# Performance work log

Measured on AMD Instinct MI355X. Metric: run time of the kernel, lower is better.

## Reference

```python
import jax, jax.numpy as jnp
import numpy as np
import math

B, L, E, H, NL, M, S, R = 4, 1024, 512, 8, 2, 2048, 256, 2
Dh = E // H
NEG = jnp.finfo(jnp.float32).min


def _posenc(n, d):
    pos = np.arange(n)[:, None].astype(np.float32)
    div = np.exp(np.arange(0, d, 2).astype(np.float32) * (-math.log(10000.0) / d))
    pe = np.zeros((n, d), np.float32)
    pe[:, 0::2] = np.sin(pos * div)
    pe[:, 1::2] = np.cos(pos * div)
    return jnp.asarray(pe)


def _temb(t, dim, max_positions=10000):
    half = dim // 2
    freqs = jnp.exp(jnp.arange(half, dtype=jnp.float32) * (-math.log(max_positions) / (half - 1)))
    a = t[:, None] * freqs[None, :]
    return jnp.concatenate([jnp.sin(a), jnp.cos(a)], axis=1)


def _ln(x, s, b, eps=1e-5):
    m = x.mean(-1, keepdims=True)
    v = jnp.mean((x - m) ** 2, axis=-1, keepdims=True)
    return (x - m) * jax.lax.rsqrt(v + eps) * s + b


def _gelu(x):
    return jax.nn.gelu(x, approximate=False)


def _block(h, W, b, lns, lnb, mW1, mb1, mW2, mb2, mask):
    # prenorm self-attention
    z = _ln(h, lns[0], lnb[0])
    q = (z @ W[0] + b[0]).reshape(B, L, H, Dh) / math.sqrt(Dh)
    k = (z @ W[1] + b[1]).reshape(B, L, H, Dh)
    v = (z @ W[2] + b[2]).reshape(B, L, H, Dh)
    logits = jnp.einsum('bqhd,bkhd->bhqk', q, k)
    att = jax.nn.softmax(jnp.where(mask, logits, NEG), axis=-1)
    o = jnp.einsum('bhqk,bkhd->bqhd', att, v).reshape(B, L, E)
    h = h + o @ W[3] + b[3]
    # prenorm feed-forward
    z = _ln(h, lns[1], lnb[1])
    return h + _gelu(z @ mW1 + mb1) @ mW2 + mb2


def setup_inputs():
    key = jax.random.key(0)
    ks = iter(jax.random.split(key, 48))
    def nrm(shape, s=0.02):
        return jax.random.normal(next(ks), shape, jnp.float32) * s
    inp = {
        'x': jax.random.randint(next(ks), (B, L), 0, S),
        't': jax.random.uniform(next(ks), (B,), jnp.float32) * 1000.0,
        'embed': nrm((S, E), 1.0),
        'attn_W': nrm((2, NL, 4, E, E)),
        'attn_b': jnp.zeros((2, NL, 4, E)),
        'ln_s': jnp.ones((2, NL, 2, E)),
        'ln_b': jnp.zeros((2, NL, 2, E)),
        'mlp_W1': nrm((2, NL, E, M)),
        'mlp_b1': jnp.zeros((2, NL, M)),
        'mlp_W2': nrm((2, NL, M, E)),
        'mlp_b2': jnp.zeros((2, NL, E)),
        'ca_Wq': nrm((E, E)),
        'ca_Wk': nrm((E, E)), 'ca_bk': jnp.zeros((E,)),
        'ca_Wv': nrm((E, E)), 'ca_bv': jnp.zeros((E,)),
        'ca_Wo': nrm((E, E)), 'ca_bo': jnp.zeros((E,)),
        'ro_ln1_s': jnp.ones((E,)), 'ro_ln1_b': jnp.zeros((E,)),
        'ro_ln2_s': jnp.ones((E,)), 'ro_ln2_b': jnp.zeros((E,)),
        'in_W': nrm((E, 2 * E)), 'in_b': jnp.zeros((2 * E,)),
        'tmlp_W1': nrm((E, M)), 'tmlp_b1': jnp.zeros((M,)),
        'tmlp_W2': nrm((M, 4 * E)), 'tmlp_b2': jnp.zeros((4 * E,)),
        'res_W1': nrm((R, 2 * E, M)), 'res_b1': jnp.zeros((R, M)),
        'res_W2': nrm((R, M, 2 * E)), 'res_b2': jnp.zeros((R, 2 * E)),
        'res_ln_s': jnp.ones((R, 2 * E)), 'res_ln_b': jnp.zeros((R, 2 * E)),
        'film_W': nrm((R, 4 * E, 4 * E)), 'film_b': jnp.ones((R, 4 * E)),
        'out_W': nrm((2 * E, S)), 'out_b': jnp.zeros((S,)),
    }
    return inp


def reference(x, t, embed, attn_W, attn_b, ln_s, ln_b, mlp_W1, mlp_b1, mlp_W2, mlp_b2,
              ca_Wq, ca_Wk, ca_bk, ca_Wv, ca_bv, ca_Wo, ca_bo,
              ro_ln1_s, ro_ln1_b, ro_ln2_s, ro_ln2_b,
              in_W, in_b, tmlp_W1, tmlp_b1, tmlp_W2, tmlp_b2,
              res_W1, res_b1, res_W2, res_b2, res_ln_s, res_ln_b,
              film_W, film_b, out_W, out_b):
    temb = _temb(t, E)                       # [B,E]
    tok = embed[x]                           # [B,L,E]
    pe = _posenc(L, E)[None]
    cond = temb[:, None, :]
    il = jnp.arange(L)
    causal = (il[None, :] <= il[:, None])[None, None]  # [1,1,L,L]
    embeds = []
    for d in range(2):
        if d == 0:  # l2r: shift right, prepend temb token, causal mask
            h = jnp.concatenate([cond, tok[:, :-1]], axis=1)
            mask = causal
        else:       # r2l: shift left, append temb token, anti-causal mask
            h = jnp.concatenate([tok[:, 1:], cond], axis=1)
            mask = jnp.swapaxes(causal, -1, -2)
        h = h + pe
        for l in range(NL):
            h = _block(h, attn_W[d, l], attn_b[d, l], ln_s[d, l], ln_b[d, l],
                       mlp_W1[d, l], mlp_b1[d, l], mlp_W2[d, l], mlp_b2[d, l], mask)
        embeds.append(h)
    l2r_embed, r2l_embed = embeds
    # AttentionReadout (prenorm) with joint-mask cross-attention
    inputs = l2r_embed + r2l_embed
    l2r_n = _ln(l2r_embed, ro_ln1_s, ro_ln1_b)
    r2l_n = _ln(r2l_embed, ro_ln2_s, ro_ln2_b)
    q = ((l2r_n + r2l_n) @ ca_Wq).reshape(B, L, H, Dh) / math.sqrt(Dh)
    allv = jnp.concatenate([temb[:, None], l2r_n, r2l_n], axis=1)  # [B,2L+1,E]
    k = (allv @ ca_Wk + ca_bk).reshape(B, 2 * L + 1, H, Dh)
    v = (allv @ ca_Wv + ca_bv).reshape(B, 2 * L + 1, H, Dh)
    logits = jnp.einsum('bqhd,bkhd->bhqk', q, k)  # [B,H,L,2L+1]
    m_l2r = il[None, :] > il[:, None]   # triu, diag=1
    m_r2l = il[None, :] < il[:, None]   # tril, diag=-1
    joint = jnp.concatenate([jnp.ones((L, 1), bool), m_l2r, m_r2l], axis=-1)[None, None]
    att = jax.nn.softmax(jnp.where(joint, logits, NEG), axis=-1)
    xat = jnp.einsum('bhqk,bkhd->bqhd', att, v).reshape(B, L, E)
    xat = xat @ ca_Wo + ca_bo + inputs
    # ResidualReadout: FiLM-conditioned residual MLP stack
    t4 = _gelu(temb @ tmlp_W1 + tmlp_b1) @ tmlp_W2 + tmlp_b2  # [B,4E]
    h = xat @ in_W + in_b                                     # [B,L,2E]
    for i in range(R):
        film = t4 @ film_W[i] + film_b[i]
        z = _gelu(h @ res_W1[i] + res_b1[i]) @ res_W2[i] + res_b2[i]
        h = _ln(h + z, res_ln_s[i], res_ln_b[i])
        fa, fb = jnp.split(film[:, None, :], 2, axis=-1)
        h = fa * h + fb
    return h @ out_W + out_b  # [B,L,S]
```

## Files before the change

kernel.cpp:

```cpp
#include <hip/hip_runtime.h>
#include <hip/hip_bf16.h>


#define NEGF -3.4028235e38f
#define LOG2E 1.4426950408889634f

using bf16x8 = __attribute__((ext_vector_type(8))) short;
using f32x4  = __attribute__((ext_vector_type(4))) float;

__device__ inline float bf2f(unsigned short u) {
    return __uint_as_float(((unsigned int)u) << 16);
}
__device__ inline unsigned short f2b(float f) {
    unsigned int u = __float_as_uint(f);
    return (unsigned short)((u + 0x7fff + ((u >> 16) & 1)) >> 16);
}

__device__ inline void gl_lds16(const void* g, void* l) {
    __builtin_amdgcn_global_load_lds(
        (const __attribute__((address_space(1))) void*)(uintptr_t)g,
        (__attribute__((address_space(3))) void*)(unsigned int)(uintptr_t)l,
        16, 0, 0);
}

template<int BM>
__global__ __launch_bounds__(256) void gemm_bf16_k(
    const unsigned short* __restrict__ A,
    const unsigned short* __restrict__ Wt0, const unsigned short* __restrict__ Wt1,
    const float* __restrict__ bias0, const float* __restrict__ bias1, int mhalf,
    const float* __restrict__ res,
    float* __restrict__ Cf, unsigned short* __restrict__ Cb,
    unsigned short* __restrict__ CbK, unsigned short* __restrict__ Ct, int ldkv,
    int M, int N, int K, float alpha, int gelu_flag, int qkv)
{
    constexpr int MF  = BM / 32;
    constexpr int NAC = BM * 4 / 256;
    __shared__ unsigned short As[2][BM * 32];
    __shared__ unsigned short Bs[2][4096];
    const int tid  = threadIdx.x;
    const int wid  = tid >> 6;
    const int lane = tid & 63;
    const int wy   = wid >> 1, wx = wid & 1;
    const int koff = lane >> 4, l16 = lane & 15;
    const int m0 = blockIdx.y * BM, n0 = blockIdx.x * 128;

    const unsigned short* Wt = (m0 < mhalf) ? Wt0 : Wt1;
    const float* bias = (m0 < mhalf) ? bias0 : bias1;

    const unsigned short* aG[NAC];
    const unsigned short* bG[2];
    #pragma unroll
    for (int i = 0; i < NAC; ++i) {
        int c = tid + i * 256;
        int r = ((c >> 6) << 4) | (c & 15), kk = ((c >> 4) & 3) << 3;
        aG[i] = A + (size_t)(m0 + r) * K + kk;
    }
    #pragma unroll
    for (int i = 0; i < 2; ++i) {
        int c = tid + i * 256;
        int r = ((c >> 6) << 4) | (c & 15), kk = ((c >> 4) & 3) << 3;
        bG[i] = Wt + (size_t)(n0 + r) * K + kk;
    }

    f32x4 acc[MF][4] = {};
    const int nk = K >> 5;

    auto stage = [&](int buf, int k0) {
        #pragma unroll
        for (int i = 0; i < NAC; ++i)
            gl_lds16(aG[i] + k0, &As[buf][(size_t)(i * 256 + wid * 64) * 8]);
        #pragma unroll
        for (int i = 0; i < 2; ++i)
            gl_lds16(bG[i] + k0, &Bs[buf][(size_t)(i * 256 + wid * 64) * 8]);
    };

    stage(0, 0);
    int cur = 0;
    for (int it = 0; it < nk; ++it) {
        if (it + 1 < nk) {
            stage(cur ^ 1, (it + 1) << 5);
            if constexpr (BM == 128)
                asm volatile("s_waitcnt vmcnt(4)" ::: "memory");
            else
                asm volatile("s_waitcnt vmcnt(3)" ::: "memory");
        } else {
            asm volatile("s_waitcnt vmcnt(0)" ::: "memory");
        }
        __builtin_amdgcn_s_barrier();

        bf16x8 af[MF], bfr[4];
        const int foff = (koff * 16 + l16) * 8;
        #pragma unroll
        for (int i = 0; i < MF; ++i)
            af[i] = *(const bf16x8*)&As[cur][(size_t)((wy * MF + i) * 64) * 8 + foff];
        #pragma unroll
        for (int j = 0; j < 4; ++j)
            bfr[j] = *(const bf16x8*)&Bs[cur][(size_t)((wx * 4 + j) * 64) * 8 + foff];
        #pragma unroll
        for (int i = 0; i < MF; ++i)
            #pragma unroll
            for (int j = 0; j < 4; ++j)
                acc[i][j] = __builtin_amdgcn_mfma_f32_16x16x32_bf16(
                    af[i], bfr[j], acc[i][j], 0, 0, 0);

        asm volatile("" ::: "memory");
        __builtin_amdgcn_s_barrier();
        cur ^= 1;
    }

    #pragma unroll
    for (int i = 0; i < MF; ++i) {
        const int rbase = m0 + wy * (MF * 16) + i * 16 + koff * 4;
        #pragma unroll
        for (int j = 0; j < 4; ++j) {
            const int gn = n0 + wx * 64 + j * 16 + l16;
            const float bs = bias ? bias[gn] : 0.f;
            if (qkv) {
                const int seg = gn >> 9, gnl = gn & 511;
                const float av = (seg == 0) ? 0.125f : 1.0f;
                unsigned short o[4];
                #pragma unroll
                for (int r = 0; r < 4; ++r) o[r] = f2b((acc[i][j][r] + bs) * av);
                if (seg == 0) {
                    #pragma unroll
                    for (int r = 0; r < 4; ++r)
                        Cb[(size_t)(rbase + r) * 512 + gnl] = o[r];
                } else if (seg == 1) {
                    #pragma unroll
                    for (int r = 0; r < 4; ++r)
                        CbK[(size_t)(rbase + r) * 512 + gnl] = o[r];
                } else {
                    const int hh = gnl >> 6, dh = gnl & 63;
                    const int bb = rbase >> 10, l0 = rbase & 1023;
                    *(ushort4*)(Ct + ((size_t)(bb * 8 + hh) * 64 + dh) * 1024 + l0) =
                        make_ushort4(o[0], o[1], o[2], o[3]);
                }
            } else {
                float vr[4];
                #pragma unroll
                for (int r = 0; r < 4; ++r) {
                    float v = (acc[i][j][r] + bs) * alpha;
                    if (gelu_flag) v = 0.5f * v * (1.0f + erff(v * 0.70710678118654752f));
                    const size_t idx = (size_t)(rbase + r) * N + gn;
                    if (res) v += res[idx];
                    if (Cf) Cf[idx] = v;
                    if (Cb) Cb[idx] = f2b(v);
                    vr[r] = v;
                }
                if (Ct) {
                    const int hh = gn >> 6, dh = gn & 63;
                    const int bb = rbase / ldkv;
                    const int l0 = rbase - bb * ldkv;
                    *(ushort4*)(Ct + ((size_t)(bb * 8 + hh) * 64 + dh) * ldkv + l0) =
                        make_ushort4(f2b(vr[0]), f2b(vr[1]), f2b(vr[2]), f2b(vr[3]));
                }
            }
        }
    }
}

__global__ __launch_bounds__(256) void wconv(
    const float* __restrict__ src, unsigned short* __restrict__ dst,
    int K, int N, long sstride, long dstride)
{
    __shared__ float t[64][65];
    const int n0 = blockIdx.x * 64, k0 = blockIdx.y * 64;
    const float* s = src + (size_t)blockIdx.z * sstride;
    unsigned short* d = dst + (size_t)blockIdx.z * dstride;
    const int tid = threadIdx.x;
    #pragma unroll
    for (int i = 0; i < 4; ++i) {
        int lin = i * 1024 + tid * 4;
        int r = lin >> 6, c = lin & 63;
        float4 v = *(const float4*)(s + (size_t)(k0 + r) * N + n0 + c);
        t[r][c] = v.x; t[r][c + 1] = v.y; t[r][c + 2] = v.z; t[r][c + 3] = v.w;
    }
    __syncthreads();
    #pragma unroll
    for (int i = 0; i < 8; ++i) {
        int lin = i * 512 + tid * 2;
        int rn = lin >> 6, ck = lin & 63;
        ushort2 o;
        o.x = f2b(t[ck][rn]); o.y = f2b(t[ck + 1][rn]);
        *(ushort2*)(d + (size_t)(n0 + rn) * K + k0 + ck) = o;
    }
}

__global__ __launch_bounds__(256) void skinny_k(
    const float* __restrict__ A, const float* __restrict__ W,
    float* __restrict__ P, int N, int K)
{
    const int n = blockIdx.x * 256 + threadIdx.x;
    const int s = blockIdx.y;
    const int k0 = s * 32;
    float a0 = 0.f, a1 = 0.f, a2 = 0.f, a3 = 0.f;
    #pragma unroll 8
    for (int k = k0; k < k0 + 32; ++k) {
        float w = W[(size_t)k * N + n];
        a0 = fmaf(A[k], w, a0);
        a1 = fmaf(A[K + k], w, a1);
        a2 = fmaf(A[2 * K + k], w, a2);
        a3 = fmaf(A[3 * K + k], w, a3);
    }
    float* p = P + (size_t)s * 4 * N;
    p[n] = a0; p[N + n] = a1; p[2 * N + n] = a2; p[3 * N + n] = a3;
}

__global__ __launch_bounds__(256) void skinny_red(
    const float* __restrict__ P, const float* __restrict__ bias,
    float* __restrict__ C, int N, int nsplit, int gelu_flag)
{
    const int n = blockIdx.x * 256 + threadIdx.x;
    const int r = blockIdx.y;
    float acc = 0.f;
    for (int s = 0; s < nsplit; ++s) acc += P[((size_t)s * 4 + r) * N + n];
    float v = acc + (bias ? bias[n] : 0.f);
    if (gelu_flag) v = 0.5f * v * (1.0f + erff(v * 0.70710678118654752f));
    C[(size_t)r * N + n] = v;
}

__global__ __launch_bounds__(256) void ln_kernel(
    const float* __restrict__ X, const float* __restrict__ X2,
    const float* __restrict__ s, const float* __restrict__ b,
    float* __restrict__ Yf, unsigned short* __restrict__ Yb,
    int D, const float* __restrict__ film, int rows_per_batch, long pstride)
{
    const int row = blockIdx.x;
    const int tid = threadIdx.x;
    const float* x = X + (size_t)row * D;
    const float* x2 = X2 ? X2 + (size_t)row * D : nullptr;
    const float* se = s + (size_t)(row >> 12) * pstride;
    const float* be = b + (size_t)(row >> 12) * pstride;

    float sum = 0.f, sq = 0.f;
    for (int c = tid; c < D; c += 256) {
        float v = x[c] + (x2 ? x2[c] : 0.f);
        sum += v; sq += v * v;
    }
    __shared__ float r1[4], r2[4];
    __shared__ float s_mean, s_rstd;
    for (int off = 32; off > 0; off >>= 1) {
        sum += __shfl_down(sum, off);
        sq  += __shfl_down(sq,  off);
    }
    if ((tid & 63) == 0) { r1[tid >> 6] = sum; r2[tid >> 6] = sq; }
    __syncthreads();
    if (tid == 0) {
        float ts = r1[0] + r1[1] + r1[2] + r1[3];
        float tq = r2[0] + r2[1] + r2[2] + r2[3];
        float mean = ts / (float)D;
        float var = tq / (float)D - mean * mean;
        s_mean = mean;
        s_rstd = rsqrtf(var + 1e-5f);
    }
    __syncthreads();
    const float mean = s_mean, rstd = s_rstd;
    const float* fa = nullptr; const float* fb = nullptr;
    if (film) {
        int batch = row / rows_per_batch;
        fa = film + (size_t)batch * 2 * D;
        fb = fa + D;
    }
    for (int c = tid; c < D; c += 256) {
        float v = x[c] + (x2 ? x2[c] : 0.f);
        float y = (v - mean) * rstd * se[c] + be[c];
        if (film) y = fa[c] * y + fb[c];
        if (Yf) Yf[(size_t)row * D + c] = y;
        if (Yb) Yb[(size_t)row * D + c] = f2b(y);
    }
}

__global__ void temb_kernel(const float* __restrict__ t, float* __restrict__ temb,
                            unsigned short* __restrict__ tembb)
{
    int b = blockIdx.x;
    int i = threadIdx.x;
    float f = expf((float)i * (-9.210340371976184f / 255.0f));
    float a = t[b] * f;
    float sv = sinf(a), cv = cosf(a);
    temb[b * 512 + i]        = sv;
    temb[b * 512 + 256 + i]  = cv;
    tembb[b * 512 + i]       = f2b(sv);
    tembb[b * 512 + 256 + i] = f2b(cv);
}

__global__ void embed_kernel(const int* __restrict__ x, const float* __restrict__ temb,
                             const float* __restrict__ embed,
                             float* __restrict__ l2r, float* __restrict__ r2l)
{
    const int i = blockIdx.x;
    const int b = blockIdx.y;
    const int d = blockIdx.z;
    float* out = (d == 0 ? l2r : r2l) + ((size_t)(b * 1024 + i) * 512);
    const float* src;
    if (d == 0) src = (i == 0)    ? temb + b * 512 : embed + (size_t)x[b * 1024 + (i - 1)] * 512;
    else        src = (i == 1023) ? temb + b * 512 : embed + (size_t)x[b * 1024 + (i + 1)] * 512;
    for (int e = threadIdx.x; e < 512; e += 256) {
        int j = e >> 1;
        float div = expf((float)(2 * j) * (-9.210340371976184f / 512.0f));
        float ang = (float)i * div;
        float pe = (e & 1) ? cosf(ang) : sinf(ang);
        out[e] = src[e] + pe;
    }
}

__global__ void add_kernel(const float* __restrict__ A, const float* __restrict__ B,
                           float* __restrict__ C, int n)
{
    int i = blockIdx.x * blockDim.x + threadIdx.x;
    int stride = gridDim.x * blockDim.x;
    for (; i < n; i += stride) C[i] = A[i] + B[i];
}

__global__ void add_bf16(const unsigned int* __restrict__ A,
                         const unsigned int* __restrict__ B,
                         unsigned int* __restrict__ C, int nwords)
{
    int i = blockIdx.x * blockDim.x + threadIdx.x;
    int stride = gridDim.x * blockDim.x;
    for (; i < nwords; i += stride) {
        unsigned int a = A[i], b = B[i];
        float lo = __uint_as_float(a << 16) + __uint_as_float(b << 16);
        float hi = __uint_as_float(a & 0xffff0000u) + __uint_as_float(b & 0xffff0000u);
        C[i] = (unsigned int)f2b(lo) | ((unsigned int)f2b(hi) << 16);
    }
}

__global__ void build_allv_b(const unsigned short* __restrict__ tembb,
                             const unsigned short* __restrict__ l2rn,
                             const unsigned short* __restrict__ r2ln,
                             unsigned short* __restrict__ allv)
{
    const int k = blockIdx.x;
    const int b = blockIdx.y;
    unsigned short* out = allv + ((size_t)b * 2080 + k) * 512;
    const unsigned short* src;
    if (k == 0)         src = tembb + b * 512;
    else if (k <= 1024) src = l2rn + ((size_t)(b * 1024 + (k - 1)) * 512);
    else                src = r2ln + ((size_t)(b * 1024 + (k - 1025)) * 512);
    ((uint4*)out)[threadIdx.x] = ((const uint4*)src)[threadIdx.x];
}

__global__ __launch_bounds__(256) void attn_mfma(
    const unsigned short* __restrict__ Q, const unsigned short* __restrict__ K,
    const unsigned short* __restrict__ Vt, unsigned short* __restrict__ O, int mode)
{
    const int E = 512;
    const int LKP = (mode == 2) ? 2080 : 1024;
    const int idf = blockIdx.x;
    const int chunk = gridDim.x >> 3;
    const int w = (idf & 7) * chunk + (idf >> 3);
    const int qt = w & 15, h = (w >> 4) & 7, bb = w >> 7;
    const int dir = (mode == 2) ? 2 : (bb >> 2);
    const int q0 = qt * 64;
    const int tid = threadIdx.x;
    const int wid = tid >> 6, lane = tid & 63;
    const int fr = lane & 15;
    const int fs = lane >> 4;
    const int wq0 = q0 + wid * 16;

    __shared__ unsigned short Qs[4096];
    __shared__ unsigned short Ks[4096];
    __shared__ unsigned short Vs[4096];
    __shared__ unsigned short Ps[4][16][72];

    {
        const unsigned short* Qbase = Q + ((size_t)bb * 1024 + q0) * E + h * 64;
        #pragma unroll
        for (int it = 0; it < 2; ++it) {
            int i = tid + it * 256;
            int r = i & 63, c = i >> 6;
            *(uint4*)&Qs[(size_t)(c * 64 + r) * 8] =
                *(const uint4*)(Qbase + (size_t)r * E + c * 8);
        }
    }
    __syncthreads();
    const bf16x8 aq0 = *(const bf16x8*)&Qs[(size_t)(fs * 64 + wid * 16 + fr) * 8];
    const bf16x8 aq1 = *(const bf16x8*)&Qs[(size_t)((fs + 4) * 64 + wid * 16 + fr) * 8];

    float m_r[4], l_r[4];
    f32x4 o_acc[4] = {};
    #pragma unroll
    for (int r = 0; r < 4; ++r) { m_r[r] = NEGF; l_r[r] = 0.f; }

    int kt0, kt1;
    if (dir == 0)      { kt0 = 0;  kt1 = qt; }
    else if (dir == 1) { kt0 = qt; kt1 = 15; }
    else               { kt0 = 0;  kt1 = 31; }

    const unsigned short* Kb0 = K + ((size_t)bb * LKP) * E + h * 64;
    const unsigned short* Vb0 = Vt + (size_t)(bb * 8 + h) * 64 * LKP;

    for (int kt = kt0; kt <= kt1; ++kt) {
        if (dir == 2) {
            if (kt >= 1 && kt <= 15 && 64 * kt + 62 <= q0) continue;
            if (kt >= 17 && 64 * kt - 1025 >= q0 + 63) continue;
        }
        const int k0 = kt * 64;

        __syncthreads();

        {
            const unsigned short* Kbase = Kb0 + (size_t)k0 * E;
            const unsigned short* Vbase = Vb0 + k0;
            #pragma unroll
            for (int it = 0; it < 2; ++it) {
                int i = tid + it * 256;
                int r = i & 63, c = i >> 6;
                *(uint4*)&Ks[(size_t)(c * 64 + r) * 8] =
                    *(const uint4*)(Kbase + (size_t)r * E + c * 8);
                *(uint4*)&Vs[(size_t)(c * 64 + r) * 8] =
                    *(const uint4*)(Vbase + (size_t)r * LKP + c * 8);
            }
        }
        __syncthreads();

        f32x4 s[4] = {};
        __builtin_amdgcn_s_setprio(1);
        #pragma unroll
        for (int t = 0; t < 4; ++t) {
            bf16x8 bk0 = *(const bf16x8*)&Ks[(size_t)(fs * 64 + t * 16 + fr) * 8];
            bf16x8 bk1 = *(const bf16x8*)&Ks[(size_t)((fs + 4) * 64 + t * 16 + fr) * 8];
            s[t] = __builtin_amdgcn_mfma_f32_16x16x32_bf16(aq0, bk0, s[t], 0, 0, 0);
            s[t] = __builtin_amdgcn_mfma_f32_16x16x32_bf16(aq1, bk1, s[t], 0, 0, 0);
        }
        __builtin_amdgcn_s_setprio(0);

        bool need_mask;
        if (dir != 2) need_mask = (kt == qt);
        else if (kt >= 1 && kt <= 15) need_mask = !((64 * kt - 1) > (q0 + 63));
        else if (kt >= 17)            need_mask = !((64 * kt + 63 - 1025) < q0);
        else                          need_mask = true;
        if (need_mask) {
            #pragma unroll
            for (int t = 0; t < 4; ++t) {
                #pragma unroll
                for (int r = 0; r < 4; ++r) {
                    int q = wq0 + fs * 4 + r;
                    int k = k0 + t * 16 + fr;
                    bool valid;
                    if (dir == 0)      valid = (k <= q);
                    else if (dir == 1) valid = (k >= q);
                    else valid = (k == 0) || (k <= 1024 ? (k - 1) > q : (k - 1025) < q);
                    if (!valid) s[t][r] = NEGF;
                }
            }
        }

        float c_[4], rs[4];
        #pragma unroll
        for (int r = 0; r < 4; ++r) {
            float v = fmaxf(fmaxf(s[0][r], s[1][r]), fmaxf(s[2][r], s[3][r]));
            v = fmaxf(v, __shfl_xor(v, 1));
            v = fmaxf(v, __shfl_xor(v, 2));
            v = fmaxf(v, __shfl_xor(v, 4));
            v = fmaxf(v, __shfl_xor(v, 8));
            float mnew = fmaxf(m_r[r], v);
            c_[r] = exp2f((m_r[r] - mnew) * LOG2E);
            m_r[r] = mnew;
            rs[r] = 0.f;
        }
        #pragma unroll
        for (int t = 0; t < 4; ++t) {
            #pragma unroll
            for (int r = 0; r < 4; ++r) {
                float p = exp2f((s[t][r] - m_r[r]) * LOG2E);
                s[t][r] = p;
                rs[r] += p;
            }
        }
        #pragma unroll
        for (int r = 0; r < 4; ++r) {
            float v = rs[r];
            v += __shfl_xor(v, 1);
            v += __shfl_xor(v, 2);
            v += __shfl_xor(v, 4);
            v += __shfl_xor(v, 8);
            l_r[r] = l_r[r] * c_[r] + v;
            o_acc[0][r] *= c_[r]; o_acc[1][r] *= c_[r];
            o_acc[2][r] *= c_[r]; o_acc[3][r] *= c_[r];
        }

        #pragma unroll
        for (int t = 0; t < 4; ++t)
            #pragma unroll
            for (int r = 0; r < 4; ++r)
                Ps[wid][fs * 4 + r][t * 16 + fr] = f2b(s[t][r]);
        __syncthreads();

        bf16x8 pa0 = *(const bf16x8*)&Ps[wid][fr][fs * 8];
        bf16x8 pa1 = *(const bf16x8*)&Ps[wid][fr][fs * 8 + 32];
        __builtin_amdgcn_s_setprio(1);
        #pragma unroll
        for (int t = 0; t < 4; ++t) {
            bf16x8 bv0 = *(const bf16x8*)&Vs[(size_t)(fs * 64 + t * 16 + fr) * 8];
            bf16x8 bv1 = *(const bf16x8*)&Vs[(size_t)((fs + 4) * 64 + t * 16 + fr) * 8];
            o_acc[t] = __builtin_amdgcn_mfma_f32_16x16x32_bf16(pa0, bv0, o_acc[t], 0, 0, 0);
            o_acc[t] = __builtin_amdgcn_mfma_f32_16x16x32_bf16(pa1, bv1, o_acc[t], 0, 0, 0);
        }
        __builtin_amdgcn_s_setprio(0);
    }

    unsigned short* Obase = O + ((size_t)bb * 1024 + q0) * E + h * 64;
    float invl[4];
    #pragma unroll
    for (int r = 0; r < 4; ++r) invl[r] = 1.f / l_r[r];
    #pragma unroll
    for (int t = 0; t < 4; ++t)
        #pragma unroll
        for (int r = 0; r < 4; ++r)
            Obase[(size_t)(wid * 16 + fs * 4 + r) * E + t * 16 + fr] =
                f2b(o_acc[t][r] * invl[r]);
}


static inline void gemmb(hipStream_t st, int BM, const unsigned short* A,
                         const unsigned short* Wt0, const unsigned short* Wt1,
                         const float* bias0, const float* bias1, int mhalf,
                         const float* res, float* Cf, unsigned short* Cb,
                         unsigned short* CbK, unsigned short* Ct, int ldkv,
                         int M, int N, int K, float alpha, int gelu, int qkv)
{
    dim3 g(N / 128, M / BM);
    if (BM == 128)
        gemm_bf16_k<128><<<g, dim3(256), 0, st>>>(A, Wt0, Wt1, bias0, bias1, mhalf,
            res, Cf, Cb, CbK, Ct, ldkv, M, N, K, alpha, gelu, qkv);
    else
        gemm_bf16_k<64><<<g, dim3(256), 0, st>>>(A, Wt0, Wt1, bias0, bias1, mhalf,
            res, Cf, Cb, CbK, Ct, ldkv, M, N, K, alpha, gelu, qkv);
}

static inline void sgemm4(hipStream_t st, const float* A, const float* W,
                          const float* bias, float* C, float* P,
                          int N, int K, int gelu)
{
    const int nsplit = K / 32;
    skinny_k<<<dim3(N / 256, nsplit), 256, 0, st>>>(A, W, P, N, K);
    skinny_red<<<dim3(N / 256, 4), 256, 0, st>>>(P, bias, C, N, nsplit, gelu);
}

extern "C" void kernel_launch(void* const* d_in, const int* in_sizes, int n_in,
                              void* d_out, int out_size, void* d_ws, size_t ws_size,
                              hipStream_t stream)
{
    const int*   x      = (const int*)  d_in[0];
    const float* t      = (const float*)d_in[1];
    const float* embedW = (const float*)d_in[2];
    const float* attn_W = (const float*)d_in[3];
    const float* attn_b = (const float*)d_in[4];
    const float* ln_s   = (const float*)d_in[5];
    const float* ln_b   = (const float*)d_in[6];
    const float* mlp_W1 = (const float*)d_in[7];
    const float* mlp_b1 = (const float*)d_in[8];
    const float* mlp_W2 = (const float*)d_in[9];
    const float* mlp_b2 = (const float*)d_in[10];
    const float* ca_Wq  = (const float*)d_in[11];
    const float* ca_Wk  = (const float*)d_in[12];
    const float* ca_bk  = (const float*)d_in[13];
    const float* ca_Wv  = (const float*)d_in[14];
    const float* ca_bv  = (const float*)d_in[15];
    const float* ca_Wo  = (const float*)d_in[16];
    const float* ca_bo  = (const float*)d_in[17];
    const float* ro1s   = (const float*)d_in[18];
    const float* ro1b   = (const float*)d_in[19];
    const float* ro2s   = (const float*)d_in[20];
    const float* ro2b   = (const float*)d_in[21];
    const float* in_W   = (const float*)d_in[22];
    const float* in_b   = (const float*)d_in[23];
    const float* tm_W1  = (const float*)d_in[24];
    const float* tm_b1  = (const float*)d_in[25];
    const float* tm_W2  = (const float*)d_in[26];
    const float* tm_b2  = (const float*)d_in[27];
    const float* res_W1 = (const float*)d_in[28];
    const float* res_b1 = (const float*)d_in[29];
    const float* res_W2 = (const float*)d_in[30];
    const float* res_b2 = (const float*)d_in[31];
    const float* rls    = (const float*)d_in[32];
    const float* rlb    = (const float*)d_in[33];
    const float* film_W = (const float*)d_in[34];
    const float* film_b = (const float*)d_in[35];
    const float* out_W  = (const float*)d_in[36];
    const float* out_b  = (const float*)d_in[37];
    float* out = (float*)d_out;
    (void)ws_size; (void)in_sizes; (void)n_in; (void)out_size;

    char* base = (char*)d_ws;
    size_t off = 0;
    auto alloc = [&](size_t bytes) -> char* {
        char* p = base + off;
        off = (off + bytes + 255) & ~(size_t)255;
        return p;
    };
    float* TEMB  = (float*)alloc(8192);
    float* TM1   = (float*)alloc(32768);
    float* T4    = (float*)alloc(32768);
    float* FILM  = (float*)alloc(32768);
    unsigned short* TEMBb = (unsigned short*)alloc(4096);
    float* SKP   = (float*)alloc(2097152);

    float* HB  = (float*)alloc(16777216);
    float* L2R = HB;
    float* R2L = HB + 4096 * 512;
    float* Z   = (float*)alloc(8388608);
    float* H2  = (float*)alloc(16777216);
    float* Z2  = (float*)alloc(16777216);

    unsigned short* Zb  = (unsigned short*)alloc(8388608);
    unsigned short* Qb  = (unsigned short*)alloc(8388608);
    unsigned short* Kb  = (unsigned short*)alloc(8388608);
    unsigned short* Vb  = (unsigned short*)alloc(8388608);
    unsigned short* Ob  = (unsigned short*)alloc(8388608);
    unsigned short* H2b = (unsigned short*)alloc(8388608);

    unsigned short* BIG = (unsigned short*)alloc(33554432);
    unsigned short* MIDb  = BIG;
    unsigned short* ALLVb = BIG;
    unsigned short* K2b   = BIG + 4259840;
    unsigned short* V2T   = BIG + 8519680;

    unsigned short* WT = (unsigned short*)alloc(45613056);
    const size_t wt_attn = 0,        wt_mlp1 = 4194304, wt_mlp2 = 8388608;
    const size_t wt_caq = 12582912,  wt_cak = 12845056, wt_cav = 13107200,
                 wt_cao = 13369344,  wt_in  = 13631488;
    const size_t wt_res1 = 14155776, wt_res2 = 18350080, wt_out = 22544384;

    wconv<<<dim3(8, 8, 16), 256, 0, stream>>>(attn_W, WT + wt_attn, 512, 512, 262144, 262144);
    wconv<<<dim3(32, 8, 4), 256, 0, stream>>>(mlp_W1, WT + wt_mlp1, 512, 2048, 1048576, 1048576);
    wconv<<<dim3(8, 32, 4), 256, 0, stream>>>(mlp_W2, WT + wt_mlp2, 2048, 512, 1048576, 1048576);
    wconv<<<dim3(8, 8), 256, 0, stream>>>(ca_Wq, WT + wt_caq, 512, 512, 0, 0);
    wconv<<<dim3(8, 8), 256, 0, stream>>>(ca_Wk, WT + wt_cak, 512, 512, 0, 0);
    wconv<<<dim3(8, 8), 256, 0, stream>>>(ca_Wv, WT + wt_cav, 512, 512, 0, 0);
    wconv<<<dim3(8, 8), 256, 0, stream>>>(ca_Wo, WT + wt_cao, 512, 512, 0, 0);
    wconv<<<dim3(16, 8), 256, 0, stream>>>(in_W, WT + wt_in, 512, 1024, 0, 0);
    wconv<<<dim3(32, 16, 2), 256, 0, stream>>>(res_W1, WT + wt_res1, 1024, 2048, 2097152, 2097152);
    wconv<<<dim3(16, 32, 2), 256, 0, stream>>>(res_W2, WT + wt_res2, 2048, 1024, 2097152, 2097152);
    wconv<<<dim3(4, 16), 256, 0, stream>>>(out_W, WT + wt_out, 1024, 256, 0, 0);

    temb_kernel<<<dim3(4), dim3(256), 0, stream>>>(t, TEMB, TEMBb);
    embed_kernel<<<dim3(1024, 4, 2), dim3(256), 0, stream>>>(x, TEMB, embedW, L2R, R2L);

    for (int l = 0; l < 2; ++l) {
        const size_t d1 = 2 + l;
        ln_kernel<<<8192, 256, 0, stream>>>(HB, nullptr,
            ln_s + (l * 2 + 0) * 512, ln_b + (l * 2 + 0) * 512,
            nullptr, Zb, 512, nullptr, 1024, 2048);
        gemmb(stream, 64, Zb,
              WT + wt_attn + (size_t)l * 1048576, WT + wt_attn + d1 * 1048576,
              attn_b + l * 2048, attn_b + d1 * 2048, 4096,
              nullptr, nullptr, Qb, Kb, Vb, 1024, 8192, 1536, 512, 1.f, 0, 1);
        attn_mfma<<<dim3(1024), dim3(256), 0, stream>>>(Qb, Kb, Vb, Ob, -1);
        gemmb(stream, 64, Ob,
              WT + wt_attn + (size_t)(l * 4 + 3) * 262144,
              WT + wt_attn + (d1 * 4 + 3) * 262144,
              attn_b + (l * 4 + 3) * 512, attn_b + (d1 * 4 + 3) * 512, 4096,
              HB, HB, nullptr, nullptr, nullptr, 1, 8192, 512, 512, 1.f, 0, 0);
        ln_kernel<<<8192, 256, 0, stream>>>(HB, nullptr,
            ln_s + (l * 2 + 1) * 512, ln_b + (l * 2 + 1) * 512,
            nullptr, Zb, 512, nullptr, 1024, 2048);
        gemmb(stream, 64, Zb,
              WT + wt_mlp1 + (size_t)l * 1048576, WT + wt_mlp1 + d1 * 1048576,
              mlp_b1 + l * 2048, mlp_b1 + d1 * 2048, 4096,
              nullptr, nullptr, MIDb, nullptr, nullptr, 1, 8192, 2048, 512, 1.f, 1, 0);
        gemmb(stream, 64, MIDb,
              WT + wt_mlp2 + (size_t)l * 1048576, WT + wt_mlp2 + d1 * 1048576,
              mlp_b2 + l * 512, mlp_b2 + d1 * 512, 4096,
              HB, HB, nullptr, nullptr, nullptr, 1, 8192, 512, 2048, 1.f, 0, 0);
    }

    add_kernel<<<2048, 256, 0, stream>>>(L2R, R2L, Z, 2097152);
    ln_kernel<<<4096, 256, 0, stream>>>(L2R, nullptr, ro1s, ro1b, nullptr, Qb, 512, nullptr, 1024, 0);
    ln_kernel<<<4096, 256, 0, stream>>>(R2L, nullptr, ro2s, ro2b, nullptr, Kb, 512, nullptr, 1024, 0);
    add_bf16<<<1024, 256, 0, stream>>>((const unsigned int*)Qb, (const unsigned int*)Kb,
                                       (unsigned int*)Vb, 1048576);
    build_allv_b<<<dim3(2049, 4), 64, 0, stream>>>(TEMBb, Qb, Kb, ALLVb);
    gemmb(stream, 64, Vb, WT + wt_caq, WT + wt_caq, nullptr, nullptr, 1 << 30,
          nullptr, nullptr, Zb, nullptr, nullptr, 1, 4096, 512, 512, 0.125f, 0, 0);
    gemmb(stream, 64, ALLVb, WT + wt_cak, WT + wt_cak, ca_bk, ca_bk, 1 << 30,
          nullptr, nullptr, K2b, nullptr, nullptr, 1, 8320, 512, 512, 1.f, 0, 0);
    gemmb(stream, 64, ALLVb, WT + wt_cav, WT + wt_cav, ca_bv, ca_bv, 1 << 30,
          nullptr, nullptr, nullptr, nullptr, V2T, 2080, 8320, 512, 512, 1.f, 0, 0);
    attn_mfma<<<dim3(512), dim3(256), 0, stream>>>(Zb, K2b, V2T, Ob, 2);
    gemmb(stream, 64, Ob, WT + wt_cao, WT + wt_cao, ca_bo, ca_bo, 1 << 30,
          Z, nullptr, Qb, nullptr, nullptr, 1, 4096, 512, 512, 1.f, 0, 0);

    sgemm4(stream, TEMB, tm_W1, tm_b1, TM1, SKP, 2048, 512, 1);
    sgemm4(stream, TM1, tm_W2, tm_b2, T4, SKP, 2048, 2048, 0);

    gemmb(stream, 64, Qb, WT + wt_in, WT + wt_in, in_b, in_b, 1 << 30,
          nullptr, H2, H2b, nullptr, nullptr, 1, 4096, 1024, 512, 1.f, 0, 0);
    for (int i = 0; i < 2; ++i) {
        sgemm4(stream, T4, film_W + (size_t)i * 4194304, film_b + i * 2048,
               FILM, SKP, 2048, 2048, 0);
        gemmb(stream, 64, H2b, WT + wt_res1 + (size_t)i * 2097152,
              WT + wt_res1 + (size_t)i * 2097152,
              res_b1 + i * 2048, res_b1 + i * 2048, 1 << 30,
              nullptr, nullptr, MIDb, nullptr, nullptr, 1, 4096, 2048, 1024, 1.f, 1, 0);
        gemmb(stream, 64, MIDb, WT + wt_res2 + (size_t)i * 2097152,
              WT + wt_res2 + (size_t)i * 2097152,
              res_b2 + i * 1024, res_b2 + i * 1024, 1 << 30,
              nullptr, Z2, nullptr, nullptr, nullptr, 1, 4096, 1024, 2048, 1.f, 0, 0);
        ln_kernel<<<4096, 256, 0, stream>>>(H2, Z2, rls + i * 1024, rlb + i * 1024,
                                            H2, H2b, 1024, FILM, 1024, 0);
    }

    gemmb(stream, 64, H2b, WT + wt_out, WT + wt_out, out_b, out_b, 1 << 30,
          nullptr, out, nullptr, nullptr, nullptr, 1, 4096, 256, 1024, 1.f, 0, 0);
}
```

Baseline: 1.136 ms.

## Triple-buffer GEMM LDS stages and register-prefetch attention K/V tiles

```diff
diff --git a/kernel.cpp b/kernel.cpp
--- a/kernel.cpp
+++ b/kernel.cpp
@@ -35,8 +35,8 @@
 {
     constexpr int MF  = BM / 32;
     constexpr int NAC = BM * 4 / 256;
-    __shared__ unsigned short As[2][BM * 32];
-    __shared__ unsigned short Bs[2][4096];
+    __shared__ unsigned short As[3][BM * 32];
+    __shared__ unsigned short Bs[3][4096];
     const int tid  = threadIdx.x;
     const int wid  = tid >> 6;
     const int lane = tid & 63;
@@ -75,16 +75,19 @@
     };
 
     stage(0, 0);
-    int cur = 0;
+    if (nk > 1) stage(1, 32);
+    int cur = 0, nxt = 2;
     for (int it = 0; it < nk; ++it) {
-        if (it + 1 < nk) {
-            stage(cur ^ 1, (it + 1) << 5);
-            if constexpr (BM == 128)
-                asm volatile("s_waitcnt vmcnt(4)" ::: "memory");
-            else
-                asm volatile("s_waitcnt vmcnt(3)" ::: "memory");
+        const int ahead = nk - 1 - it;
+        if (ahead >= 2) stage(nxt, (it + 2) << 5);
+        if constexpr (BM == 128) {
+            if (ahead >= 2)      asm volatile("s_waitcnt vmcnt(8)" ::: "memory");
+            else if (ahead == 1) asm volatile("s_waitcnt vmcnt(4)" ::: "memory");
+            else                 asm volatile("s_waitcnt vmcnt(0)" ::: "memory");
         } else {
-            asm volatile("s_waitcnt vmcnt(0)" ::: "memory");
+            if (ahead >= 2)      asm volatile("s_waitcnt vmcnt(6)" ::: "memory");
+            else if (ahead == 1) asm volatile("s_waitcnt vmcnt(3)" ::: "memory");
+            else                 asm volatile("s_waitcnt vmcnt(0)" ::: "memory");
         }
         __builtin_amdgcn_s_barrier();
 
@@ -105,7 +108,8 @@
 
         asm volatile("" ::: "memory");
         __builtin_amdgcn_s_barrier();
-        cur ^= 1;
+        cur = (cur == 2) ? 0 : cur + 1;
+        nxt = (nxt == 2) ? 0 : nxt + 1;
     }
 
     #pragma unroll
@@ -383,37 +387,49 @@
     #pragma unroll
     for (int r = 0; r < 4; ++r) { m_r[r] = NEGF; l_r[r] = 0.f; }
 
-    int kt0, kt1;
-    if (dir == 0)      { kt0 = 0;  kt1 = qt; }
-    else if (dir == 1) { kt0 = qt; kt1 = 15; }
-    else               { kt0 = 0;  kt1 = 31; }
+    int nt, ktA = 1;
+    if (dir == 0)      nt = qt + 1;
+    else if (dir == 1) nt = 16 - qt;
+    else { ktA = (qt >= 1) ? qt : 1; nt = 1 + (qt + 16 - ktA + 1); }
+    auto kt_of = [&](int j) -> int {
+        if (dir == 0) return j;
+        if (dir == 1) return qt + j;
+        return (j == 0) ? 0 : (ktA + j - 1);
+    };
 
     const unsigned short* Kb0 = K + ((size_t)bb * LKP) * E + h * 64;
     const unsigned short* Vb0 = Vt + (size_t)(bb * 8 + h) * 64 * LKP;
 
-    for (int kt = kt0; kt <= kt1; ++kt) {
-        if (dir == 2) {
-            if (kt >= 1 && kt <= 15 && 64 * kt + 62 <= q0) continue;
-            if (kt >= 17 && 64 * kt - 1025 >= q0 + 63) continue;
-        }
+    const int sr = tid & 63, sc = tid >> 6;
+    auto load_tile = [&](int kt, uint4* kr, uint4* vr) {
+        const unsigned short* Kbase = Kb0 + (size_t)(kt * 64) * E;
+        const unsigned short* Vbase = Vb0 + kt * 64;
+        #pragma unroll
+        for (int it = 0; it < 2; ++it) {
+            kr[it] = *(const uint4*)(Kbase + (size_t)sr * E + (sc + it * 4) * 8);
+            vr[it] = *(const uint4*)(Vbase + (size_t)sr * LKP + (sc + it * 4) * 8);
+        }
+    };
+
+    uint4 kr[2], vr[2];
+    load_tile(kt_of(0), kr, vr);
+
+    for (int j = 0; j < nt; ++j) {
+        const int kt = kt_of(j);
         const int k0 = kt * 64;
 
-        __syncthreads();
-
-        {
-            const unsigned short* Kbase = Kb0 + (size_t)k0 * E;
-            const unsigned short* Vbase = Vb0 + k0;
-            #pragma unroll
-            for (int it = 0; it < 2; ++it) {
-                int i = tid + it * 256;
-                int r = i & 63, c = i >> 6;
-                *(uint4*)&Ks[(size_t)(c * 64 + r) * 8] =
-                    *(const uint4*)(Kbase + (size_t)r * E + c * 8);
-                *(uint4*)&Vs[(size_t)(c * 64 + r) * 8] =
-                    *(const uint4*)(Vbase + (size_t)r * LKP + c * 8);
-            }
-        }
-        __syncthreads();
+        asm volatile("s_waitcnt lgkmcnt(0)" ::: "memory");
+        __builtin_amdgcn_s_barrier();
+
+        #pragma unroll
+        for (int it = 0; it < 2; ++it) {
+            *(uint4*)&Ks[(size_t)((sc + it * 4) * 64 + sr) * 8] = kr[it];
+            *(uint4*)&Vs[(size_t)((sc + it * 4) * 64 + sr) * 8] = vr[it];
+        }
+        if (j + 1 < nt) load_tile(kt_of(j + 1), kr, vr);
+
+        asm volatile("s_waitcnt lgkmcnt(0)" ::: "memory");
+        __builtin_amdgcn_s_barrier();
 
         f32x4 s[4] = {};
         __builtin_amdgcn_s_setprio(1);
@@ -486,7 +502,6 @@
             #pragma unroll
             for (int r = 0; r < 4; ++r)
                 Ps[wid][fs * 4 + r][t * 16 + fr] = f2b(s[t][r]);
-        __syncthreads();
 
         bf16x8 pa0 = *(const bf16x8*)&Ps[wid][fr][fs * 8];
         bf16x8 pa1 = *(const bf16x8*)&Ps[wid][fr][fs * 8 + 32];
```

Measured after the change: 1.211 ms. 1.07x slower.
